# Kernel tuning notes

Measured on AMD Instinct MI355X. Metric: run time of the kernel, lower is better.

The kernel has to match this reference:

```python
import jax, jax.numpy as jnp
import numpy as np
import math

B, T, C = 2, 2048, 2048
H, KV, HD = 16, 4, 128  # num_heads, num_kv_heads, head_dim
REP = H // KV


def _rope_tables(T, hd, base=10000.0):
    inv_freq = 1.0 / (base ** (np.arange(0, hd, 2, dtype=np.float32) / hd))  # [hd/2]
    t = np.arange(T, dtype=np.float32)
    freqs = np.outer(t, inv_freq)                 # [T, hd/2]
    emb = np.concatenate([freqs, freqs], axis=-1)  # [T, hd]
    return jnp.asarray(np.cos(emb)), jnp.asarray(np.sin(emb))


def setup_inputs() -> dict:
    key = jax.random.key(0)
    ks = jax.random.split(key, 5)
    cos, sin = _rope_tables(T, HD)
    std = 0.02
    return {
        "x": jax.random.normal(ks[0], (B, T, C), dtype=jnp.float32),
        "cos": cos,
        "sin": sin,
        "Wq": jax.random.normal(ks[1], (C, H * HD), dtype=jnp.float32) * std,
        "Wk": jax.random.normal(ks[2], (C, KV * HD), dtype=jnp.float32) * std,
        "Wv": jax.random.normal(ks[3], (C, KV * HD), dtype=jnp.float32) * std,
        "Wo": jax.random.normal(ks[4], (H * HD, C), dtype=jnp.float32) * std,
    }


def _rotate_half(t):
    h = t.shape[-1] // 2
    return jnp.concatenate([-t[..., h:], t[..., :h]], axis=-1)


def reference(x, cos, sin, Wq, Wk, Wv, Wo):
    Bx, Tx, Cx = x.shape
    q = (x @ Wq).reshape(Bx, Tx, H, HD).transpose(0, 2, 1, 3)   # [B,H,T,hd]
    k = (x @ Wk).reshape(Bx, Tx, KV, HD).transpose(0, 2, 1, 3)  # [B,KV,T,hd]
    v = (x @ Wv).reshape(Bx, Tx, KV, HD).transpose(0, 2, 1, 3)
    c = cos[None, None]  # [1,1,T,hd]
    s = sin[None, None]
    q = q * c + _rotate_half(q) * s
    k = k * c + _rotate_half(k) * s
    # repeat_kv: expand KV heads to H heads (interleave within groups)
    k = jnp.repeat(k, REP, axis=1)  # [B,H,T,hd]
    v = jnp.repeat(v, REP, axis=1)
    scores = jnp.einsum("bhqd,bhkd->bhqk", q, k) / math.sqrt(HD)
    causal = jnp.triu(jnp.full((Tx, Tx), float("-inf"), dtype=scores.dtype), k=1)
    scores = jax.nn.softmax(scores + causal[None, None], axis=-1)
    out = jnp.einsum("bhqk,bhkd->bhqd", scores, v)  # [B,H,T,hd]
    out = out.transpose(0, 2, 1, 3).reshape(Bx, Tx, H * HD)
    return out @ Wo
```

## Files before the change

### kernel.cpp

```cpp
#include <hip/hip_runtime.h>
#include <hip/hip_bf16.h>
#include <math.h>

typedef __bf16 bf16_t;
typedef __bf16 bf16x8 __attribute__((ext_vector_type(8)));
typedef float f32x4 __attribute__((ext_vector_type(4)));

constexpr int Bc = 2, Tc = 2048, Cdim = 2048, Hc = 16, KVc = 4, HDc = 128;
constexpr int Mc = Bc * Tc;
constexpr int Nqkv = 3072;

typedef const __attribute__((address_space(1))) void* as1_cptr;
typedef __attribute__((address_space(3))) void* as3_ptr;

__device__ __forceinline__ void gload_lds16(const bf16_t* g, bf16_t* l) {
  __builtin_amdgcn_global_load_lds((as1_cptr)(const void*)g, (as3_ptr)(void*)l, 16, 0, 0);
}

__device__ __forceinline__ unsigned int cvt_pk_bf16(float lo, float hi) {
  unsigned int r;
  asm("v_cvt_pk_bf16_f32 %0, %1, %2" : "=v"(r) : "v"(lo), "v"(hi));
  return r;
}
__device__ __forceinline__ void perm32swap(unsigned int& a, unsigned int& b) {
  asm("v_permlane32_swap_b32 %0, %1" : "+v"(a), "+v"(b));
}
__device__ __forceinline__ void perm16swap(unsigned int& a, unsigned int& b) {
  asm("v_permlane16_swap_b32 %0, %1" : "+v"(a), "+v"(b));
}

__global__ void k_prep(const float* __restrict__ x, bf16_t* __restrict__ xb,
                       const float* __restrict__ Wq, const float* __restrict__ Wk,
                       const float* __restrict__ Wv, const float* __restrict__ Wo,
                       bf16_t* __restrict__ Wqt, bf16_t* __restrict__ Wkt,
                       bf16_t* __restrict__ Wvt, bf16_t* __restrict__ Wot) {
  __shared__ alignas(16) bf16_t tile[64][72];
  int bid = blockIdx.x;
  if (bid < 4096) {
    int i = (bid * 256 + threadIdx.x) * 8;
    float4 a = *(const float4*)(x + i);
    float4 b = *(const float4*)(x + i + 4);
    bf16x8 v;
    v[0] = (bf16_t)a.x; v[1] = (bf16_t)a.y; v[2] = (bf16_t)a.z; v[3] = (bf16_t)a.w;
    v[4] = (bf16_t)b.x; v[5] = (bf16_t)b.y; v[6] = (bf16_t)b.z; v[7] = (bf16_t)b.w;
    *(bf16x8*)(xb + i) = v;
    return;
  }
  bid -= 4096;
  const float* W; bf16_t* Wt; int K, N, k0, n0;
  if (bid < 1024)      { W = Wq; Wt = Wqt; K = 2048; N = 2048; k0 = (bid >> 5) * 64; n0 = (bid & 31) * 64; }
  else if (bid < 1280) { bid -= 1024; W = Wk; Wt = Wkt; K = 2048; N = 512; k0 = (bid >> 3) * 64; n0 = (bid & 7) * 64; }
  else if (bid < 1536) { bid -= 1280; W = Wv; Wt = Wvt; K = 2048; N = 512; k0 = (bid >> 3) * 64; n0 = (bid & 7) * 64; }
  else                 { bid -= 1536; W = Wo; Wt = Wot; K = 2048; N = 2048; k0 = (bid >> 5) * 64; n0 = (bid & 31) * 64; }
  const int t = threadIdx.x;
#pragma unroll
  for (int i = 0; i < 4; ++i) {
    int idx = t + i * 256;
    int r = idx >> 4;
    int c4 = (idx & 15) * 4;
    float4 v = *(const float4*)(W + (size_t)(k0 + r) * N + n0 + c4);
    tile[r][c4 + 0] = (bf16_t)v.x; tile[r][c4 + 1] = (bf16_t)v.y;
    tile[r][c4 + 2] = (bf16_t)v.z; tile[r][c4 + 3] = (bf16_t)v.w;
  }
  __syncthreads();
#pragma unroll
  for (int i = 0; i < 4; ++i) {
    int idx = t + i * 256;
    int n = idx >> 4;
    int kc = (idx & 15) * 4;
    alignas(8) bf16_t o[4];
#pragma unroll
    for (int j = 0; j < 4; ++j) o[j] = tile[kc + j][n];
    *(uint2*)(Wt + (size_t)(n0 + n) * K + k0 + kc) = *(uint2*)o;
  }
}

__global__ __launch_bounds__(256, 2) void k_gemm_bt(
    const bf16_t* __restrict__ A, const bf16_t* __restrict__ Bt,
    float* __restrict__ Cout, int M, int N, int K) {
  __shared__ alignas(16) bf16_t Ash[128 * 64];
  __shared__ alignas(16) bf16_t Bsh[128 * 64];
  const int tid = threadIdx.x;
  const int wave = tid >> 6, lane = tid & 63;
  const int col = lane & 15, quad = lane >> 4;
  const int m0 = blockIdx.y * 128, n0 = blockIdx.x * 128;
  const int wr = wave >> 1, wc = wave & 1;

  f32x4 acc[4][4];
#pragma unroll
  for (int i = 0; i < 4; ++i)
#pragma unroll
    for (int j = 0; j < 4; ++j) acc[i][j] = f32x4{0.f, 0.f, 0.f, 0.f};

  const int lrow = lane >> 3;
  const int lkc8 = (lane & 7) ^ lrow;

  for (int k0 = 0; k0 < K; k0 += 64) {
    __syncthreads();
#pragma unroll
    for (int i = 0; i < 4; ++i) {
      const int rb = wave * 32 + i * 8;
      gload_lds16(A + (size_t)(m0 + rb + lrow) * K + k0 + lkc8 * 8, Ash + rb * 64);
      gload_lds16(Bt + (size_t)(n0 + rb + lrow) * K + k0 + lkc8 * 8, Bsh + rb * 64);
    }
    __syncthreads();
#pragma unroll
    for (int kc = 0; kc < 2; ++kc) {
      bf16x8 af[4], bfr[4];
#pragma unroll
      for (int mt = 0; mt < 4; ++mt) {
        const int m = wr * 64 + mt * 16 + col;
        const int slot = (kc * 4 + quad) ^ (m & 7);
        af[mt] = *(const bf16x8*)(Ash + m * 64 + slot * 8);
      }
#pragma unroll
      for (int nt = 0; nt < 4; ++nt) {
        const int n = wc * 64 + nt * 16 + col;
        const int slot = (kc * 4 + quad) ^ (n & 7);
        bfr[nt] = *(const bf16x8*)(Bsh + n * 64 + slot * 8);
      }
#pragma unroll
      for (int mt = 0; mt < 4; ++mt)
#pragma unroll
        for (int nt = 0; nt < 4; ++nt)
          acc[mt][nt] = __builtin_amdgcn_mfma_f32_16x16x32_bf16(
              af[mt], bfr[nt], acc[mt][nt], 0, 0, 0);
    }
  }
#pragma unroll
  for (int mt = 0; mt < 4; ++mt)
#pragma unroll
    for (int i = 0; i < 4; ++i) {
      const int row = m0 + wr * 64 + mt * 16 + quad * 4 + i;
#pragma unroll
      for (int nt = 0; nt < 4; ++nt)
        Cout[(size_t)row * N + n0 + wc * 64 + nt * 16 + col] = acc[mt][nt][i];
    }
}

__global__ __launch_bounds__(256, 2) void k_gemm_qkv(
    const bf16_t* __restrict__ A, const bf16_t* __restrict__ Bt,
    const float* __restrict__ cs, const float* __restrict__ sn,
    bf16_t* __restrict__ Qp, bf16_t* __restrict__ Kp, bf16_t* __restrict__ Vt) {
  constexpr int K = Cdim;
  __shared__ alignas(16) bf16_t Ash[128 * 64];
  __shared__ alignas(16) bf16_t Bsh[128 * 64];
  const int tid = threadIdx.x;
  const int wave = tid >> 6, lane = tid & 63;
  const int col = lane & 15, quad = lane >> 4;
  const int m0 = blockIdx.y * 128, n0 = blockIdx.x * 128;

  f32x4 acc[2][8];
#pragma unroll
  for (int i = 0; i < 2; ++i)
#pragma unroll
    for (int j = 0; j < 8; ++j) acc[i][j] = f32x4{0.f, 0.f, 0.f, 0.f};

  const int lrow = lane >> 3;
  const int lkc8 = (lane & 7) ^ lrow;

  for (int k0 = 0; k0 < K; k0 += 64) {
    __syncthreads();
#pragma unroll
    for (int i = 0; i < 4; ++i) {
      const int rb = wave * 32 + i * 8;
      gload_lds16(A + (size_t)(m0 + rb + lrow) * K + k0 + lkc8 * 8, Ash + rb * 64);
      gload_lds16(Bt + (size_t)(n0 + rb + lrow) * K + k0 + lkc8 * 8, Bsh + rb * 64);
    }
    __syncthreads();
#pragma unroll
    for (int kc = 0; kc < 2; ++kc) {
      bf16x8 af[2], bfr[8];
#pragma unroll
      for (int mt = 0; mt < 2; ++mt) {
        const int m = wave * 32 + mt * 16 + col;
        const int slot = (kc * 4 + quad) ^ (m & 7);
        af[mt] = *(const bf16x8*)(Ash + m * 64 + slot * 8);
      }
#pragma unroll
      for (int nt = 0; nt < 8; ++nt) {
        const int n = nt * 16 + col;
        const int slot = (kc * 4 + quad) ^ (n & 7);
        bfr[nt] = *(const bf16x8*)(Bsh + n * 64 + slot * 8);
      }
#pragma unroll
      for (int mt = 0; mt < 2; ++mt)
#pragma unroll
        for (int nt = 0; nt < 8; ++nt)
          acc[mt][nt] = __builtin_amdgcn_mfma_f32_16x16x32_bf16(
              af[mt], bfr[nt], acc[mt][nt], 0, 0, 0);
    }
  }

  const int bx = n0 >> 7;
  if (bx < 20) {
    const bool isQ = bx < 16;
#pragma unroll
    for (int mt = 0; mt < 2; ++mt)
#pragma unroll
      for (int i = 0; i < 4; ++i) {
        const int row = m0 + wave * 32 + mt * 16 + quad * 4 + i;
        const int b = row >> 11, t = row & (Tc - 1);
        bf16_t* op = isQ ? Qp + ((size_t)(b * Hc + bx) * Tc + t) * HDc
                         : Kp + ((size_t)(b * KVc + (bx - 16)) * Tc + t) * HDc;
        const float* cr = cs + t * HDc;
        const float* sr = sn + t * HDc;
#pragma unroll
        for (int nt = 0; nt < 4; ++nt) {
          const int d = nt * 16 + col;
          const float c = cr[d], s = sr[d];
          const float x0 = acc[mt][nt][i], x1 = acc[mt][nt + 4][i];
          op[d]      = (bf16_t)(x0 * c - x1 * s);
          op[d + 64] = (bf16_t)(x1 * c + x0 * s);
        }
      }
  } else {
    const int kv = bx - 20;
#pragma unroll
    for (int mt = 0; mt < 2; ++mt) {
      const int row0 = m0 + wave * 32 + mt * 16 + quad * 4;
      const int b = row0 >> 11, t0 = row0 & (Tc - 1);
#pragma unroll
      for (int nt = 0; nt < 8; ++nt) {
        const int d = nt * 16 + col;
        alignas(8) bf16_t o[4];
#pragma unroll
        for (int i = 0; i < 4; ++i) o[i] = (bf16_t)acc[mt][nt][i];
        *(uint2*)(Vt + ((size_t)(b * KVc + kv) * HDc + d) * Tc + t0) = *(uint2*)o;
      }
    }
  }
}

__global__ __launch_bounds__(256, 2) void k_attn(
    const bf16_t* __restrict__ Qp, const bf16_t* __restrict__ Kp,
    const bf16_t* __restrict__ Vt, bf16_t* __restrict__ Oout) {
  constexpr float sc2 = 0.08838834764831845f * 1.4426950408889634f;
  __shared__ alignas(16) bf16_t Ksh[2][64 * 128];
  __shared__ alignas(16) bf16_t Vsh[2][128 * 64];

  const int i2 = blockIdx.x, h = blockIdx.y, b = blockIdx.z;
  const int kvh = h >> 2;
  const int tid = threadIdx.x, wave = tid >> 6, lane = tid & 63;
  const int col = lane & 15, quad = lane >> 4;

  const bf16_t* Kb = Kp + (size_t)(b * KVc + kvh) * Tc * HDc;
  const bf16_t* Vb = Vt + (size_t)(b * KVc + kvh) * HDc * Tc;
  const bf16_t* Qbh = Qp + (size_t)(b * Hc + h) * Tc * HDc;

  const int st_kr = lane >> 4, st_kc8 = lane & 15;
  const int st_vr = lane >> 3, st_vc8 = lane & 7;

  const int qb0 = 31 - i2, qb1 = i2;
  const int n0it = qb0 + 1;
  const int ntot = qb0 + qb1 + 2;

  int q0 = qb0 * 64 + wave * 16;
  const int qr = wave * 16 + col;

  bf16x8 qf[4];
  {
    const bf16_t* qbase = Qbh + (size_t)(q0 + col) * HDc;
#pragma unroll
    for (int kc = 0; kc < 4; ++kc) {
      bf16x8 raw = *(const bf16x8*)(qbase + kc * 32 + quad * 8);
#pragma unroll
      for (int e = 0; e < 8; ++e) qf[kc][e] = (bf16_t)((float)raw[e] * sc2);
    }
  }

  f32x4 o_acc[8];
#pragma unroll
  for (int nb = 0; nb < 8; ++nb) o_acc[nb] = f32x4{0.f, 0.f, 0.f, 0.f};
  float l_i = 0.f;

#pragma unroll
  for (int i = 0; i < 4; ++i) {
    const int rb = wave * 16 + i * 4;
    const int r = rb + st_kr;
    const int kc8 = st_kc8 ^ (r & 7);
    gload_lds16(Kb + (size_t)r * HDc + kc8 * 8, &Ksh[0][rb * 128]);
    const int db = wave * 32 + i * 8;
    const int d = db + st_vr;
    const int tc8 = st_vc8 ^ (d & 7);
    gload_lds16(Vb + (size_t)d * Tc + tc8 * 8, &Vsh[0][db * 64]);
  }

#pragma unroll 1
  for (int j = 0; j < ntot; ++j) {
    const int cur = j & 1;
    const bool diag = (j == qb0) || (j == ntot - 1);
    asm volatile("s_barrier" ::: "memory");
    {
      const int jn = (j + 1 < ntot) ? (j + 1) : (ntot - 1);
      const int tn = (jn < n0it) ? jn : (jn - n0it);
      const int kbn = tn * 64;
#pragma unroll
      for (int i = 0; i < 4; ++i) {
        const int rb = wave * 16 + i * 4;
        const int r = rb + st_kr;
        const int kc8 = st_kc8 ^ (r & 7);
        gload_lds16(Kb + (size_t)(kbn + r) * HDc + kc8 * 8, &Ksh[cur ^ 1][rb * 128]);
        const int db = wave * 32 + i * 8;
        const int d = db + st_vr;
        const int tc8 = st_vc8 ^ (d & 7);
        gload_lds16(Vb + (size_t)d * Tc + kbn + tc8 * 8, &Vsh[cur ^ 1][db * 64]);
      }
    }
    asm volatile("s_waitcnt vmcnt(8)" ::: "memory");
    asm volatile("s_barrier" ::: "memory");

    const bf16_t* Kc = &Ksh[cur][0];
    const bf16_t* Vc = &Vsh[cur][0];

    f32x4 st[4];
#pragma unroll
    for (int tb = 0; tb < 4; ++tb) st[tb] = f32x4{0.f, 0.f, 0.f, 0.f};
#pragma unroll
    for (int kc = 0; kc < 4; ++kc)
#pragma unroll
      for (int tb = 0; tb < 4; ++tb) {
        const int r = tb * 16 + col;
        const int slot = (kc * 4 + quad) ^ (r & 7);
        bf16x8 kf = *(const bf16x8*)(Kc + r * 128 + slot * 8);
        st[tb] = __builtin_amdgcn_mfma_f32_16x16x32_bf16(kf, qf[kc], st[tb], 0, 0, 0);
      }

    unsigned int pwrd[4][2];
#pragma unroll
    for (int tb = 0; tb < 4; ++tb) {
      const int kvb = tb * 16 + quad * 4;
      float e0 = exp2f(st[tb][0]), e1 = exp2f(st[tb][1]);
      float e2 = exp2f(st[tb][2]), e3 = exp2f(st[tb][3]);
      if (diag) {
        e0 = (kvb + 0 > qr) ? 0.f : e0;
        e1 = (kvb + 1 > qr) ? 0.f : e1;
        e2 = (kvb + 2 > qr) ? 0.f : e2;
        e3 = (kvb + 3 > qr) ? 0.f : e3;
      }
      l_i += (e0 + e1) + (e2 + e3);
      pwrd[tb][0] = cvt_pk_bf16(e0, e1);
      pwrd[tb][1] = cvt_pk_bf16(e2, e3);
    }

#pragma unroll
    for (int kc = 0; kc < 2; ++kc) {
      unsigned int a0 = pwrd[2 * kc][0], b0 = pwrd[2 * kc + 1][0];
      unsigned int a1 = pwrd[2 * kc][1], b1 = pwrd[2 * kc + 1][1];
      perm32swap(a0, b0);
      perm32swap(a1, b1);
      perm16swap(a0, b0);
      perm16swap(a1, b1);
      union { unsigned int w[4]; bf16x8 v; } u;
      u.w[0] = a0; u.w[1] = a1; u.w[2] = b0; u.w[3] = b1;
      const bf16x8 pf = u.v;
#pragma unroll
      for (int nb = 0; nb < 8; ++nb) {
        const int d = nb * 16 + col;
        const int vslot = (kc * 4 + quad) ^ (d & 7);
        bf16x8 vf = *(const bf16x8*)(Vc + d * 64 + vslot * 8);
        o_acc[nb] = __builtin_amdgcn_mfma_f32_16x16x32_bf16(pf, vf, o_acc[nb], 0, 0, 0);
      }
    }

    if (j == qb0) {
      float rs = l_i;
      rs += __shfl_xor(rs, 16);
      rs += __shfl_xor(rs, 32);
      const float inv = 1.0f / rs;
#pragma unroll
      for (int i = 0; i < 4; ++i) {
        const float iq = __shfl(inv, quad * 4 + i);
        const int qrow = q0 + quad * 4 + i;
        bf16_t* op = Oout + ((size_t)(b * Tc) + qrow) * (Hc * HDc) + h * HDc;
#pragma unroll
        for (int nb = 0; nb < 8; ++nb) op[nb * 16 + col] = (bf16_t)(o_acc[nb][i] * iq);
      }
      l_i = 0.f;
#pragma unroll
      for (int nb = 0; nb < 8; ++nb) o_acc[nb] = f32x4{0.f, 0.f, 0.f, 0.f};
      q0 = qb1 * 64 + wave * 16;
      const bf16_t* qbase = Qbh + (size_t)(q0 + col) * HDc;
#pragma unroll
      for (int kc = 0; kc < 4; ++kc) {
        bf16x8 raw = *(const bf16x8*)(qbase + kc * 32 + quad * 8);
#pragma unroll
        for (int e = 0; e < 8; ++e) qf[kc][e] = (bf16_t)((float)raw[e] * sc2);
      }
    }
  }

  {
    float rs = l_i;
    rs += __shfl_xor(rs, 16);
    rs += __shfl_xor(rs, 32);
    const float inv = 1.0f / rs;
#pragma unroll
    for (int i = 0; i < 4; ++i) {
      const float iq = __shfl(inv, quad * 4 + i);
      const int qrow = q0 + quad * 4 + i;
      bf16_t* op = Oout + ((size_t)(b * Tc) + qrow) * (Hc * HDc) + h * HDc;
#pragma unroll
      for (int nb = 0; nb < 8; ++nb) op[nb * 16 + col] = (bf16_t)(o_acc[nb][i] * iq);
    }
  }
}

extern "C" void kernel_launch(void* const* d_in, const int* in_sizes, int n_in,
                              void* d_out, int out_size, void* d_ws, size_t ws_size,
                              hipStream_t stream) {
  (void)in_sizes; (void)n_in; (void)out_size; (void)ws_size;
  const float* x    = (const float*)d_in[0];
  const float* cosT = (const float*)d_in[1];
  const float* sinT = (const float*)d_in[2];
  const float* Wq   = (const float*)d_in[3];
  const float* Wk   = (const float*)d_in[4];
  const float* Wv   = (const float*)d_in[5];
  const float* Wo   = (const float*)d_in[6];
  float* out = (float*)d_out;

  char* ws = (char*)d_ws;
  size_t off = 0;
  auto take = [&](size_t bytes) { char* p = ws + off; off += (bytes + 255) & ~(size_t)255; return p; };

  bf16_t* xb    = (bf16_t*)take((size_t)Mc * Cdim * 2);
  bf16_t* Wqkvt = (bf16_t*)take((size_t)Nqkv * Cdim * 2);
  bf16_t* Wot   = (bf16_t*)take((size_t)Cdim * (Hc * HDc) * 2);
  bf16_t* Qp    = (bf16_t*)take((size_t)Mc * (Hc * HDc) * 2);
  bf16_t* Kp    = (bf16_t*)take((size_t)Mc * (KVc * HDc) * 2);
  bf16_t* Vt    = (bf16_t*)take((size_t)Mc * (KVc * HDc) * 2);
  bf16_t* Wqt = Wqkvt;
  bf16_t* Wkt = Wqkvt + (size_t)2048 * Cdim;
  bf16_t* Wvt = Wqkvt + (size_t)2560 * Cdim;
  bf16_t* attn = xb;

  k_prep<<<dim3(4096 + 1024 + 256 + 256 + 1024), dim3(256), 0, stream>>>(
      x, xb, Wq, Wk, Wv, Wo, Wqt, Wkt, Wvt, Wot);
  k_gemm_qkv<<<dim3(Nqkv / 128, Mc / 128), dim3(256), 0, stream>>>(
      xb, Wqkvt, cosT, sinT, Qp, Kp, Vt);
  k_attn<<<dim3(16, Hc, Bc), dim3(256), 0, stream>>>(Qp, Kp, Vt, attn);
  k_gemm_bt<<<dim3(Cdim / 128, Mc / 128), dim3(256), 0, stream>>>(
      attn, Wot, out, Mc, Cdim, Hc * HDc);
}
```

Before: 287.4 us.

## Process two 16-row query groups per wave in attention to double K/V reuse

Each wave of the attention kernel now computes 32 query rows (two MFMA groups) against each K/V tile staged in LDS, so a block covers 128 queries. The grid is halved and the causal tile pairing is adjusted to 128-row query tiles with absolute-index masking on the two diagonal KV tiles. This raises MFMA work per LDS load and per K/V fetch. In exchange it uses more registers, runs one block per CU, and has fewer blocks to fill the device.

```diff
diff --git a/kernel.cpp b/kernel.cpp
--- a/kernel.cpp
+++ b/kernel.cpp
@@ -232,7 +232,7 @@
   }
 }
 
-__global__ __launch_bounds__(256, 2) void k_attn(
+__global__ __launch_bounds__(256, 1) void k_attn(
     const bf16_t* __restrict__ Qp, const bf16_t* __restrict__ Kp,
     const bf16_t* __restrict__ Vt, bf16_t* __restrict__ Oout) {
   constexpr float sc2 = 0.08838834764831845f * 1.4426950408889634f;
@@ -251,28 +251,35 @@
   const int st_kr = lane >> 4, st_kc8 = lane & 15;
   const int st_vr = lane >> 3, st_vc8 = lane & 7;
 
-  const int qb0 = 31 - i2, qb1 = i2;
-  const int n0it = qb0 + 1;
-  const int ntot = qb0 + qb1 + 2;
-
-  int q0 = qb0 * 64 + wave * 16;
-  const int qr = wave * 16 + col;
-
-  bf16x8 qf[4];
+  const int qt0 = 15 - i2, qt1 = i2;
+  const int n0it = 2 * (qt0 + 1);
+  const int ntot = n0it + 2 * (qt1 + 1);
+
+  int q0 = qt0 * 128 + wave * 32;
+
+  bf16x8 qfA[4], qfB[4];
   {
-    const bf16_t* qbase = Qbh + (size_t)(q0 + col) * HDc;
+    const bf16_t* qa = Qbh + (size_t)(q0 + col) * HDc;
+    const bf16_t* qb = Qbh + (size_t)(q0 + 16 + col) * HDc;
 #pragma unroll
     for (int kc = 0; kc < 4; ++kc) {
-      bf16x8 raw = *(const bf16x8*)(qbase + kc * 32 + quad * 8);
-#pragma unroll
-      for (int e = 0; e < 8; ++e) qf[kc][e] = (bf16_t)((float)raw[e] * sc2);
-    }
-  }
-
-  f32x4 o_acc[8];
-#pragma unroll
-  for (int nb = 0; nb < 8; ++nb) o_acc[nb] = f32x4{0.f, 0.f, 0.f, 0.f};
-  float l_i = 0.f;
+      bf16x8 ra = *(const bf16x8*)(qa + kc * 32 + quad * 8);
+      bf16x8 rb = *(const bf16x8*)(qb + kc * 32 + quad * 8);
+#pragma unroll
+      for (int e = 0; e < 8; ++e) {
+        qfA[kc][e] = (bf16_t)((float)ra[e] * sc2);
+        qfB[kc][e] = (bf16_t)((float)rb[e] * sc2);
+      }
+    }
+  }
+
+  f32x4 o_accA[8], o_accB[8];
+#pragma unroll
+  for (int nb = 0; nb < 8; ++nb) {
+    o_accA[nb] = f32x4{0.f, 0.f, 0.f, 0.f};
+    o_accB[nb] = f32x4{0.f, 0.f, 0.f, 0.f};
+  }
+  float l_iA = 0.f, l_iB = 0.f;
 
 #pragma unroll
   for (int i = 0; i < 4; ++i) {
@@ -289,12 +296,14 @@
 #pragma unroll 1
   for (int j = 0; j < ntot; ++j) {
     const int cur = j & 1;
-    const bool diag = (j == qb0) || (j == ntot - 1);
+    const int tn = (j < n0it) ? j : (j - n0it);
+    const int kb = tn * 64;
+    const bool diag = (j >= n0it - 2 && j < n0it) || (j >= ntot - 2);
     asm volatile("s_barrier" ::: "memory");
     {
       const int jn = (j + 1 < ntot) ? (j + 1) : (ntot - 1);
-      const int tn = (jn < n0it) ? jn : (jn - n0it);
-      const int kbn = tn * 64;
+      const int tnn = (jn < n0it) ? jn : (jn - n0it);
+      const int kbn = tnn * 64;
 #pragma unroll
       for (int i = 0; i < 4; ++i) {
         const int rb = wave * 16 + i * 4;
@@ -313,9 +322,12 @@
     const bf16_t* Kc = &Ksh[cur][0];
     const bf16_t* Vc = &Vsh[cur][0];
 
-    f32x4 st[4];
-#pragma unroll
-    for (int tb = 0; tb < 4; ++tb) st[tb] = f32x4{0.f, 0.f, 0.f, 0.f};
+    f32x4 stA[4], stB[4];
+#pragma unroll
+    for (int tb = 0; tb < 4; ++tb) {
+      stA[tb] = f32x4{0.f, 0.f, 0.f, 0.f};
+      stB[tb] = f32x4{0.f, 0.f, 0.f, 0.f};
+    }
 #pragma unroll
     for (int kc = 0; kc < 4; ++kc)
 #pragma unroll
@@ -323,85 +335,117 @@
         const int r = tb * 16 + col;
         const int slot = (kc * 4 + quad) ^ (r & 7);
         bf16x8 kf = *(const bf16x8*)(Kc + r * 128 + slot * 8);
-        st[tb] = __builtin_amdgcn_mfma_f32_16x16x32_bf16(kf, qf[kc], st[tb], 0, 0, 0);
-      }
-
-    unsigned int pwrd[4][2];
+        stA[tb] = __builtin_amdgcn_mfma_f32_16x16x32_bf16(kf, qfA[kc], stA[tb], 0, 0, 0);
+        stB[tb] = __builtin_amdgcn_mfma_f32_16x16x32_bf16(kf, qfB[kc], stB[tb], 0, 0, 0);
+      }
+
+    unsigned int pwA[4][2], pwB[4][2];
+    const int qrA = q0 + col, qrB = q0 + 16 + col;
 #pragma unroll
     for (int tb = 0; tb < 4; ++tb) {
-      const int kvb = tb * 16 + quad * 4;
-      float e0 = exp2f(st[tb][0]), e1 = exp2f(st[tb][1]);
-      float e2 = exp2f(st[tb][2]), e3 = exp2f(st[tb][3]);
+      const int kvb = kb + tb * 16 + quad * 4;
+      float a0 = exp2f(stA[tb][0]), a1 = exp2f(stA[tb][1]);
+      float a2 = exp2f(stA[tb][2]), a3 = exp2f(stA[tb][3]);
+      float b0 = exp2f(stB[tb][0]), b1 = exp2f(stB[tb][1]);
+      float b2 = exp2f(stB[tb][2]), b3 = exp2f(stB[tb][3]);
       if (diag) {
-        e0 = (kvb + 0 > qr) ? 0.f : e0;
-        e1 = (kvb + 1 > qr) ? 0.f : e1;
-        e2 = (kvb + 2 > qr) ? 0.f : e2;
-        e3 = (kvb + 3 > qr) ? 0.f : e3;
-      }
-      l_i += (e0 + e1) + (e2 + e3);
-      pwrd[tb][0] = cvt_pk_bf16(e0, e1);
-      pwrd[tb][1] = cvt_pk_bf16(e2, e3);
+        a0 = (kvb + 0 > qrA) ? 0.f : a0;
+        a1 = (kvb + 1 > qrA) ? 0.f : a1;
+        a2 = (kvb + 2 > qrA) ? 0.f : a2;
+        a3 = (kvb + 3 > qrA) ? 0.f : a3;
+        b0 = (kvb + 0 > qrB) ? 0.f : b0;
+        b1 = (kvb + 1 > qrB) ? 0.f : b1;
+        b2 = (kvb + 2 > qrB) ? 0.f : b2;
+        b3 = (kvb + 3 > qrB) ? 0.f : b3;
+      }
+      l_iA += (a0 + a1) + (a2 + a3);
+      l_iB += (b0 + b1) + (b2 + b3);
+      pwA[tb][0] = cvt_pk_bf16(a0, a1);
+      pwA[tb][1] = cvt_pk_bf16(a2, a3);
+      pwB[tb][0] = cvt_pk_bf16(b0, b1);
+      pwB[tb][1] = cvt_pk_bf16(b2, b3);
     }
 
 #pragma unroll
     for (int kc = 0; kc < 2; ++kc) {
-      unsigned int a0 = pwrd[2 * kc][0], b0 = pwrd[2 * kc + 1][0];
-      unsigned int a1 = pwrd[2 * kc][1], b1 = pwrd[2 * kc + 1][1];
-      perm32swap(a0, b0);
-      perm32swap(a1, b1);
-      perm16swap(a0, b0);
-      perm16swap(a1, b1);
-      union { unsigned int w[4]; bf16x8 v; } u;
-      u.w[0] = a0; u.w[1] = a1; u.w[2] = b0; u.w[3] = b1;
-      const bf16x8 pf = u.v;
+      unsigned int a0 = pwA[2 * kc][0], c0 = pwA[2 * kc + 1][0];
+      unsigned int a1 = pwA[2 * kc][1], c1 = pwA[2 * kc + 1][1];
+      perm32swap(a0, c0); perm32swap(a1, c1);
+      perm16swap(a0, c0); perm16swap(a1, c1);
+      union { unsigned int w[4]; bf16x8 v; } uA;
+      uA.w[0] = a0; uA.w[1] = a1; uA.w[2] = c0; uA.w[3] = c1;
+      unsigned int d0 = pwB[2 * kc][0], e0 = pwB[2 * kc + 1][0];
+      unsigned int d1 = pwB[2 * kc][1], e1 = pwB[2 * kc + 1][1];
+      perm32swap(d0, e0); perm32swap(d1, e1);
+      perm16swap(d0, e0); perm16swap(d1, e1);
+      union { unsigned int w[4]; bf16x8 v; } uB;
+      uB.w[0] = d0; uB.w[1] = d1; uB.w[2] = e0; uB.w[3] = e1;
+      const bf16x8 pfA = uA.v, pfB = uB.v;
 #pragma unroll
       for (int nb = 0; nb < 8; ++nb) {
         const int d = nb * 16 + col;
         const int vslot = (kc * 4 + quad) ^ (d & 7);
         bf16x8 vf = *(const bf16x8*)(Vc + d * 64 + vslot * 8);
-        o_acc[nb] = __builtin_amdgcn_mfma_f32_16x16x32_bf16(pf, vf, o_acc[nb], 0, 0, 0);
-      }
-    }
-
-    if (j == qb0) {
-      float rs = l_i;
-      rs += __shfl_xor(rs, 16);
-      rs += __shfl_xor(rs, 32);
-      const float inv = 1.0f / rs;
-#pragma unroll
-      for (int i = 0; i < 4; ++i) {
-        const float iq = __shfl(inv, quad * 4 + i);
-        const int qrow = q0 + quad * 4 + i;
-        bf16_t* op = Oout + ((size_t)(b * Tc) + qrow) * (Hc * HDc) + h * HDc;
-#pragma unroll
-        for (int nb = 0; nb < 8; ++nb) op[nb * 16 + col] = (bf16_t)(o_acc[nb][i] * iq);
-      }
-      l_i = 0.f;
-#pragma unroll
-      for (int nb = 0; nb < 8; ++nb) o_acc[nb] = f32x4{0.f, 0.f, 0.f, 0.f};
-      q0 = qb1 * 64 + wave * 16;
-      const bf16_t* qbase = Qbh + (size_t)(q0 + col) * HDc;
+        o_accA[nb] = __builtin_amdgcn_mfma_f32_16x16x32_bf16(pfA, vf, o_accA[nb], 0, 0, 0);
+        o_accB[nb] = __builtin_amdgcn_mfma_f32_16x16x32_bf16(pfB, vf, o_accB[nb], 0, 0, 0);
+      }
+    }
+
+    if (j == n0it - 1) {
+#pragma unroll
+      for (int g = 0; g < 2; ++g) {
+        float rs = g ? l_iB : l_iA;
+        rs += __shfl_xor(rs, 16);
+        rs += __shfl_xor(rs, 32);
+        const float inv = 1.0f / rs;
+        const f32x4* oa = g ? o_accB : o_accA;
+        const int qbase = q0 + g * 16;
+#pragma unroll
+        for (int i = 0; i < 4; ++i) {
+          const float iq = __shfl(inv, quad * 4 + i);
+          const int qrow = qbase + quad * 4 + i;
+          bf16_t* op = Oout + ((size_t)(b * Tc) + qrow) * (Hc * HDc) + h * HDc;
+#pragma unroll
+          for (int nb = 0; nb < 8; ++nb) op[nb * 16 + col] = (bf16_t)(oa[nb][i] * iq);
+        }
+      }
+      l_iA = 0.f; l_iB = 0.f;
+#pragma unroll
+      for (int nb = 0; nb < 8; ++nb) {
+        o_accA[nb] = f32x4{0.f, 0.f, 0.f, 0.f};
+        o_accB[nb] = f32x4{0.f, 0.f, 0.f, 0.f};
+      }
+      q0 = qt1 * 128 + wave * 32;
+      const bf16_t* qa = Qbh + (size_t)(q0 + col) * HDc;
+      const bf16_t* qb = Qbh + (size_t)(q0 + 16 + col) * HDc;
 #pragma unroll
       for (int kc = 0; kc < 4; ++kc) {
-        bf16x8 raw = *(const bf16x8*)(qbase + kc * 32 + quad * 8);
-#pragma unroll
-        for (int e = 0; e < 8; ++e) qf[kc][e] = (bf16_t)((float)raw[e] * sc2);
-      }
-    }
-  }
-
-  {
-    float rs = l_i;
+        bf16x8 ra = *(const bf16x8*)(qa + kc * 32 + quad * 8);
+        bf16x8 rb = *(const bf16x8*)(qb + kc * 32 + quad * 8);
+#pragma unroll
+        for (int e = 0; e < 8; ++e) {
+          qfA[kc][e] = (bf16_t)((float)ra[e] * sc2);
+          qfB[kc][e] = (bf16_t)((float)rb[e] * sc2);
+        }
+      }
+    }
+  }
+
+#pragma unroll
+  for (int g = 0; g < 2; ++g) {
+    float rs = g ? l_iB : l_iA;
     rs += __shfl_xor(rs, 16);
     rs += __shfl_xor(rs, 32);
     const float inv = 1.0f / rs;
+    const f32x4* oa = g ? o_accB : o_accA;
+    const int qbase = q0 + g * 16;
 #pragma unroll
     for (int i = 0; i < 4; ++i) {
       const float iq = __shfl(inv, quad * 4 + i);
-      const int qrow = q0 + quad * 4 + i;
+      const int qrow = qbase + quad * 4 + i;
       bf16_t* op = Oout + ((size_t)(b * Tc) + qrow) * (Hc * HDc) + h * HDc;
 #pragma unroll
-      for (int nb = 0; nb < 8; ++nb) op[nb * 16 + col] = (bf16_t)(o_acc[nb][i] * iq);
+      for (int nb = 0; nb < 8; ++nb) op[nb * 16 + col] = (bf16_t)(oa[nb][i] * iq);
     }
   }
 }
@@ -438,7 +482,7 @@
       x, xb, Wq, Wk, Wv, Wo, Wqt, Wkt, Wvt, Wot);
   k_gemm_qkv<<<dim3(Nqkv / 128, Mc / 128), dim3(256), 0, stream>>>(
       xb, Wqkvt, cosT, sinT, Qp, Kp, Vt);
-  k_attn<<<dim3(16, Hc, Bc), dim3(256), 0, stream>>>(Qp, Kp, Vt, attn);
+  k_attn<<<dim3(8, Hc, Bc), dim3(256), 0, stream>>>(Qp, Kp, Vt, attn);
   k_gemm_bt<<<dim3(Cdim / 128, Mc / 128), dim3(256), 0, stream>>>(
       attn, Wot, out, Mc, Cdim, Hc * HDc);
 }
```

After: 302.5 us. 5.3% more time.
